# Performance work log

Hardware: AMD Instinct MI355X
Metric: run time of the kernel (lower is better)

The kernel has to match this reference:

```python
import jax, jax.numpy as jnp
import numpy as np

DIM = 4096
N_HEADS = 32
N_KV_HEADS = 8
HEAD_DIM = 128
WINDOW = 1024
SEQ = 2048
ROPE_THETA = 10000.0


def setup_inputs() -> dict:
    key = jax.random.key(0)
    ks = jax.random.split(key, 5)
    x = jax.random.normal(ks[0], (SEQ, DIM), dtype=jnp.float32)
    # torch nn.Linear weights are [out_features, in_features]
    wq = jax.random.normal(ks[1], (N_HEADS * HEAD_DIM, DIM), dtype=jnp.float32) * (DIM ** -0.5)
    wk = jax.random.normal(ks[2], (N_KV_HEADS * HEAD_DIM, DIM), dtype=jnp.float32) * (DIM ** -0.5)
    wv = jax.random.normal(ks[3], (N_KV_HEADS * HEAD_DIM, DIM), dtype=jnp.float32) * (DIM ** -0.5)
    wo = jax.random.normal(ks[4], (DIM, N_HEADS * HEAD_DIM), dtype=jnp.float32) * ((N_HEADS * HEAD_DIM) ** -0.5)
    # RoPE freqs: freqs_cis[t, i] = exp(1j * t * theta^(-2i/d)); store cos/sin
    inv_freq = ROPE_THETA ** (-jnp.arange(0, HEAD_DIM, 2, dtype=jnp.float32) / HEAD_DIM)  # [D/2]
    angles = jnp.arange(SEQ, dtype=jnp.float32)[:, None] * inv_freq[None, :]  # [S, D/2]
    return {"x": x, "wq": wq, "wk": wk, "wv": wv, "wo": wo,
            "cos": jnp.cos(angles), "sin": jnp.sin(angles)}


def _apply_rope(t, cos, sin):
    # t: [S, H, D]; cos/sin: [S, D/2] -> rotate consecutive pairs as complex mul
    S, H, D = t.shape
    tr = t.reshape(S, H, D // 2, 2)
    t0, t1 = tr[..., 0], tr[..., 1]
    c = cos[:, None, :]
    s = sin[:, None, :]
    out = jnp.stack([t0 * c - t1 * s, t0 * s + t1 * c], axis=-1)
    return out.reshape(S, H, D)


def reference(x, wq, wk, wv, wo, cos, sin):
    S = x.shape[0]
    repeats = N_HEADS // N_KV_HEADS
    scale = HEAD_DIM ** -0.5
    q = (x @ wq.T).reshape(S, N_HEADS, HEAD_DIM)
    k = (x @ wk.T).reshape(S, N_KV_HEADS, HEAD_DIM)
    v = (x @ wv.T).reshape(S, N_KV_HEADS, HEAD_DIM)
    q = _apply_rope(q, cos, sin)
    k = _apply_rope(k, cos, sin)
    # repeat_kv: repeat_interleave along head axis (GQA)
    k = jnp.repeat(k, repeats, axis=1)  # [S, H, D]
    v = jnp.repeat(v, repeats, axis=1)
    scores = jnp.einsum('qhd,khd->hqk', q, k) * scale  # [H, S, S]
    # sliding-window causal mask: attend to j in (i - WINDOW, i]
    i = jnp.arange(S)[:, None]
    j = jnp.arange(S)[None, :]
    allowed = (j <= i) & (i - j < WINDOW)  # [S, S]
    scores = jnp.where(allowed[None, :, :], scores, jnp.finfo(scores.dtype).min)
    probs = jax.nn.softmax(scores, axis=-1)
    out = jnp.einsum('hqk,khd->qhd', probs, v).reshape(S, N_HEADS * HEAD_DIM)
    return out @ wo.T
```

## Files before the change

kernel.cpp:

```cpp
#include <hip/hip_runtime.h>

#define DIM 4096
#define NH 32
#define NKV 8
#define HD 128
#define WINDOW 1024
#define SEQ 2048
#define QLD 6144

typedef unsigned int uint32;
typedef __attribute__((ext_vector_type(8))) short short8_t;
typedef __attribute__((ext_vector_type(8))) __bf16 bf16x8_t;
typedef __attribute__((ext_vector_type(4))) float floatx4_t;

__device__ __forceinline__ uint32 f2bf_bits(float f) {
  uint32 u = __builtin_bit_cast(uint32, f);
  return (u + 0x7fffu + ((u >> 16) & 1u)) >> 16;
}
__device__ __forceinline__ float bf2f(unsigned short b) {
  return __builtin_bit_cast(float, ((uint32)b) << 16);
}

template <class X, class Y> struct same_t { static constexpr bool v = false; };
template <class X> struct same_t<X, X> { static constexpr bool v = true; };

__device__ __forceinline__ void load_lds16(const unsigned short* g, unsigned short* l) {
  __builtin_amdgcn_global_load_lds((__attribute__((address_space(1))) void*)g,
                                   (__attribute__((address_space(3))) void*)l, 16, 0, 0);
}

template <typename TC, bool ROPE, int BM, int BN>
__global__ __launch_bounds__(512, 2) void gemm_pipe(const unsigned short* __restrict__ A,
                                                    const unsigned short* __restrict__ B,
                                                    TC* __restrict__ C, int N, int K,
                                                    const float* __restrict__ cosp,
                                                    const float* __restrict__ sinp,
                                                    int rope_ncols) {
  constexpr int BK = 32;
  constexpr int MI = BM / 32;
  constexpr int NJ = BN / 64;
  constexpr int IA = (BM * 64) / 8192;
  constexpr int IT = IA + 2;
  constexpr int AE = BM * BK;
  constexpr int BUFE = 14336;
  __shared__ unsigned short lds[3 * BUFE];

  const int tid = threadIdx.x;
  const int w = tid >> 6, lane = tid & 63;
  const int quad = lane >> 4, l16 = lane & 15;
  const int wm = w >> 2, wn = w & 3;
  const size_t m0 = (size_t)blockIdx.y * BM, n0 = (size_t)blockIdx.x * BN;

  const unsigned short* asrc[IA];
  const unsigned short* bsrc[2];
#pragma unroll
  for (int ii = 0; ii < IA; ii++) {
    const int rloc = ii * 128 + (tid >> 2);
    const int c = ((tid & 3) + 4 - ((rloc >> 1) & 3)) & 3;
    asrc[ii] = A + (m0 + rloc) * (size_t)K + c * 8;
  }
#pragma unroll
  for (int ii = 0; ii < 2; ii++) {
    const int r0 = ii ? (BN - 128) : 0;
    const int rloc = r0 + (tid >> 2);
    const int c = ((tid & 3) + 4 - ((rloc >> 1) & 3)) & 3;
    bsrc[ii] = B + (n0 + rloc) * (size_t)K + c * 8;
  }
  const int bdst1 = AE + (BN - 128) * BK;

  int aoff[MI], boff[NJ];
#pragma unroll
  for (int i = 0; i < MI; i++) {
    const int row = wm * (BM / 2) + i * 16 + l16;
    const int s = (quad + (row >> 1)) & 3;
    aoff[i] = row * BK + s * 8;
  }
#pragma unroll
  for (int j = 0; j < NJ; j++) {
    const int row = wn * (BN / 4) + j * 16 + l16;
    const int s = (quad + (row >> 1)) & 3;
    boff[j] = AE + row * BK + s * 8;
  }

  auto stage = [&](int kt, int bi) {
    unsigned short* buf = lds + bi * BUFE + w * 512;
    const size_t ko = (size_t)kt * BK;
#pragma unroll
    for (int ii = 0; ii < IA; ii++)
      load_lds16(asrc[ii] + ko, buf + ii * 4096);
    load_lds16(bsrc[0] + ko, buf + AE);
    load_lds16(bsrc[1] + ko, buf + bdst1);
  };

  floatx4_t acc[MI][NJ] = {};
  const int nt = K >> 5;

  stage(0, 0);
  stage(1, 1);
  int rb = 0;
  for (int t = 0; t < nt; t++) {
    int sb = rb + 2; if (sb >= 3) sb -= 3;
    if (t + 2 < nt) {
      stage(t + 2, sb);
      if constexpr (IT == 4) asm volatile("s_waitcnt vmcnt(8)" ::: "memory");
      else                   asm volatile("s_waitcnt vmcnt(6)" ::: "memory");
    } else if (t + 2 == nt) {
      if constexpr (IT == 4) asm volatile("s_waitcnt vmcnt(4)" ::: "memory");
      else                   asm volatile("s_waitcnt vmcnt(3)" ::: "memory");
    } else {
      asm volatile("s_waitcnt vmcnt(0)" ::: "memory");
    }
    __builtin_amdgcn_s_barrier();
    const unsigned short* buf = lds + rb * BUFE;
    bf16x8_t afr[MI], bfr[NJ];
#pragma unroll
    for (int i = 0; i < MI; i++)
      afr[i] = __builtin_bit_cast(bf16x8_t, *(const short8_t*)(buf + aoff[i]));
#pragma unroll
    for (int j = 0; j < NJ; j++)
      bfr[j] = __builtin_bit_cast(bf16x8_t, *(const short8_t*)(buf + boff[j]));
    asm volatile("s_waitcnt lgkmcnt(0)" ::: "memory");
    __builtin_amdgcn_s_barrier();
    __builtin_amdgcn_s_setprio(1);
#pragma unroll
    for (int i = 0; i < MI; i++)
#pragma unroll
      for (int j = 0; j < NJ; j++)
        acc[i][j] = __builtin_amdgcn_mfma_f32_16x16x32_bf16(afr[i], bfr[j], acc[i][j], 0, 0, 0);
    __builtin_amdgcn_s_setprio(0);
    rb = (rb == 2) ? 0 : rb + 1;
  }

#pragma unroll
  for (int i = 0; i < MI; i++)
#pragma unroll
    for (int j = 0; j < NJ; j++) {
      const int colb = (int)n0 + wn * (BN / 4) + j * 16;
      const bool do_rope = ROPE && (colb < rope_ncols);
#pragma unroll
      for (int r = 0; r < 4; r++) {
        size_t row = m0 + wm * (BM / 2) + i * 16 + quad * 4 + r;
        size_t col = n0 + wn * (BN / 4) + j * 16 + l16;
        float v = acc[i][j][r];
        if constexpr (ROPE) {
          if (do_rope) {
            float pv = __shfl_xor(v, 1);
            const int d = ((int)col & 127) >> 1;
            const float c = cosp[row * 64 + d];
            const float s = sinp[row * 64 + d];
            v = ((int)col & 1) ? (pv * s + v * c) : (v * c - pv * s);
          }
        }
        if constexpr (same_t<TC, float>::v)
          C[row * (size_t)N + col] = v;
        else
          C[row * (size_t)N + col] = (unsigned short)f2bf_bits(v);
      }
    }
}

__global__ __launch_bounds__(256) void cvt4_kernel(const float* __restrict__ s0,
                                                   const float* __restrict__ s1,
                                                   const float* __restrict__ s2,
                                                   const float* __restrict__ s3,
                                                   unsigned short* __restrict__ d0,
                                                   unsigned short* __restrict__ d1,
                                                   unsigned short* __restrict__ d2,
                                                   unsigned short* __restrict__ d3) {
  const int b = blockIdx.x;
  const float* src;
  unsigned short* dst;
  int rb;
  if (b < 4096)        { src = s0; dst = d0; rb = b; }
  else if (b < 12288)  { src = s1; dst = d1; rb = b - 4096; }
  else if (b < 14336)  { src = s2; dst = d2; rb = b - 12288; }
  else                 { src = s3; dst = d3; rb = b - 14336; }
  const int idx = rb * 256 + threadIdx.x;
  const float4* p = (const float4*)src + (size_t)idx * 2;
  float4 a = p[0], bb = p[1];
  uint32 w0 = f2bf_bits(a.x) | (f2bf_bits(a.y) << 16);
  uint32 w1 = f2bf_bits(a.z) | (f2bf_bits(a.w) << 16);
  uint32 w2 = f2bf_bits(bb.x) | (f2bf_bits(bb.y) << 16);
  uint32 w3 = f2bf_bits(bb.z) | (f2bf_bits(bb.w) << 16);
  ((uint4*)dst)[idx] = make_uint4(w0, w1, w2, w3);
}

__global__ __launch_bounds__(256) void epi_kernel(const float* __restrict__ wo,
                                                  unsigned short* __restrict__ wob,
                                                  const unsigned short* __restrict__ v,
                                                  unsigned short* __restrict__ vT) {
  __shared__ unsigned short t[64][72];
  const int b = blockIdx.x;
  const int tid = threadIdx.x;
  if (b < 8192) {
    const int idx = b * 256 + tid;
    const float4* p = (const float4*)wo + (size_t)idx * 2;
    float4 a = p[0], bb = p[1];
    uint32 w0 = f2bf_bits(a.x) | (f2bf_bits(a.y) << 16);
    uint32 w1 = f2bf_bits(a.z) | (f2bf_bits(a.w) << 16);
    uint32 w2 = f2bf_bits(bb.x) | (f2bf_bits(bb.y) << 16);
    uint32 w3 = f2bf_bits(bb.z) | (f2bf_bits(bb.w) << 16);
    ((uint4*)wob)[idx] = make_uint4(w0, w1, w2, w3);
    return;
  }
  const int bx = b - 8192;
  const int r0 = (bx & 15) * 64, s0 = (bx >> 4) * 64;
#pragma unroll
  for (int it = 0; it < 2; it++) {
    int f = it * 256 + tid;
    int si = f >> 3, cj = (f & 7) << 3;
    *(short8_t*)(&t[si][cj]) = *(const short8_t*)(v + (size_t)(s0 + si) * QLD + r0 + cj);
  }
  __syncthreads();
#pragma unroll
  for (int it = 0; it < 2; it++) {
    int f = it * 256 + tid;
    int ri = f >> 3, sj = (f & 7) << 3;
    short8_t o;
#pragma unroll
    for (int jj = 0; jj < 8; jj++) o[jj] = t[sj + jj][ri];
    *(short8_t*)(vT + (size_t)(r0 + ri) * SEQ + s0 + sj) = o;
  }
}

__global__ __launch_bounds__(512, 4) void attn_kernel(const unsigned short* __restrict__ qb,
                                                      const unsigned short* __restrict__ kb,
                                                      const unsigned short* __restrict__ vT,
                                                      unsigned short* __restrict__ attn_out) {
  const int h = blockIdx.x;
  const int qt = 15 - blockIdx.y;
  const int kvh = h >> 2;
  const int q0 = qt * 128;
  const int tid = threadIdx.x;
  const int w = tid >> 6, lane = tid & 63;
  const int quad = lane >> 4, l16 = lane & 15;
  const float SCALE = 0.08838834764831845f;

  __shared__ unsigned short Ks[64 * 128];
  __shared__ unsigned short VTs[128 * 64];
  __shared__ unsigned short PTs[8 * 16 * 72];

  unsigned short* pt = &PTs[w * 1152];

  const int krow = tid >> 4;
  const int kc16 = tid & 15;
  const int kgcol = (kc16 ^ (krow & 7)) << 3;
  const unsigned short* kgbase = kb + (size_t)krow * QLD + kvh * 128 + kgcol;
  const int vrow = tid >> 3;
  const int vc8 = tid & 7;
  const int vgcol = (vc8 ^ (vrow & 7)) << 3;
  const unsigned short* vgbase = vT + (size_t)(kvh * 128 + vrow) * 2048 + vgcol;
  unsigned short* ldsK = Ks + w * 512;
  unsigned short* ldsV = VTs + w * 512;

  bf16x8_t aq[4];
  {
    const unsigned short* qp = qb + (size_t)(q0 + w * 16 + l16) * QLD + h * 128 + quad * 8;
#pragma unroll
    for (int ks = 0; ks < 4; ks++)
      aq[ks] = __builtin_bit_cast(bf16x8_t, *(const short8_t*)(qp + ks * 32));
  }

  floatx4_t O[8] = {};
  float m_run[4], l_run[4];
#pragma unroll
  for (int r = 0; r < 4; r++) { m_run[r] = -3e38f; l_run[r] = 0.0f; }

  const int qmin = q0 + w * 16, qmax = qmin + 15;
  int kbeg = q0 - (WINDOW - 1); if (kbeg < 0) kbeg = 0;
  const int c0 = kbeg & ~63;
  const int nch = (q0 + 128 - c0) >> 6;
  const int sa = l16 & 7;

  for (int ci = 0; ci < nch; ci++) {
    const int kb0 = c0 + (ci << 6);
#pragma unroll
    for (int i = 0; i < 2; i++)
      load_lds16(kgbase + (size_t)(kb0 + i * 32) * QLD, ldsK + i * 4096);
#pragma unroll
    for (int i = 0; i < 2; i++)
      load_lds16(vgbase + kb0 + (size_t)(i * 64) * 2048, ldsV + i * 4096);
    __syncthreads();
    const bool alive = (kb0 <= qmax) && (kb0 + 63 >= qmin - (WINDOW - 1));
    if (alive) {
      floatx4_t S[4];
      __builtin_amdgcn_s_setprio(1);
#pragma unroll
      for (int j = 0; j < 4; j++) {
        floatx4_t acc = {};
        const int keyrow = j * 16 + l16;
#pragma unroll
        for (int ks = 0; ks < 4; ks++) {
          const int c16 = ((ks << 2) | quad) ^ sa;
          bf16x8_t bfk = __builtin_bit_cast(bf16x8_t,
              *(const short8_t*)(&Ks[keyrow * 128 + c16 * 8]));
          acc = __builtin_amdgcn_mfma_f32_16x16x32_bf16(aq[ks], bfk, acc, 0, 0, 0);
        }
        S[j] = acc;
      }
      __builtin_amdgcn_s_setprio(0);
      const bool need_mask = (kb0 + 63 > qmin) || (qmax - kb0 >= WINDOW);
      if (need_mask) {
#pragma unroll
        for (int j = 0; j < 4; j++) {
          const int key = kb0 + j * 16 + l16;
#pragma unroll
          for (int r = 0; r < 4; r++) {
            const int i = qmin + quad * 4 + r;
            const bool ok = (key <= i) && (i - key < WINDOW);
            S[j][r] = ok ? S[j][r] : -3e38f;
          }
        }
      }
      float mx[4], rs[4], alpha[4];
#pragma unroll
      for (int r = 0; r < 4; r++) {
        float m = S[0][r];
#pragma unroll
        for (int j = 1; j < 4; j++) m = fmaxf(m, S[j][r]);
#pragma unroll
        for (int d = 1; d < 16; d <<= 1) m = fmaxf(m, __shfl_xor(m, d, 16));
        mx[r] = fmaxf(m_run[r], m);
        alpha[r] = __expf(SCALE * (m_run[r] - mx[r]));
        m_run[r] = mx[r];
        rs[r] = 0.0f;
      }
#pragma unroll
      for (int j = 0; j < 4; j++) {
        float p[4];
#pragma unroll
        for (int r = 0; r < 4; r++) {
          const float sv = S[j][r];
          float e = __expf(SCALE * (sv - mx[r]));
          if (need_mask) e = (sv < -1e37f) ? 0.0f : e;
          p[r] = e;
          rs[r] += e;
        }
#pragma unroll
        for (int r = 0; r < 4; r++)
          pt[(quad * 4 + r) * 72 + j * 16 + l16] = (unsigned short)f2bf_bits(p[r]);
      }
#pragma unroll
      for (int r = 0; r < 4; r++) {
#pragma unroll
        for (int d = 1; d < 16; d <<= 1) rs[r] += __shfl_xor(rs[r], d, 16);
        l_run[r] = l_run[r] * alpha[r] + rs[r];
      }
#pragma unroll
      for (int nt = 0; nt < 8; nt++)
#pragma unroll
        for (int r = 0; r < 4; r++) O[nt][r] *= alpha[r];
      asm volatile("" ::: "memory");
      __builtin_amdgcn_s_setprio(1);
#pragma unroll
      for (int ks = 0; ks < 2; ks++) {
        bf16x8_t af = __builtin_bit_cast(bf16x8_t,
            *(const short8_t*)(&pt[l16 * 72 + ks * 32 + quad * 8]));
#pragma unroll
        for (int nt = 0; nt < 8; nt++) {
          const int c8 = (((ks << 2) | quad) ^ sa);
          bf16x8_t bfv = __builtin_bit_cast(bf16x8_t,
              *(const short8_t*)(&VTs[(nt * 16 + l16) * 64 + c8 * 8]));
          O[nt] = __builtin_amdgcn_mfma_f32_16x16x32_bf16(af, bfv, O[nt], 0, 0, 0);
        }
      }
      __builtin_amdgcn_s_setprio(0);
    }
    __syncthreads();
  }
  float inv_l[4];
#pragma unroll
  for (int r = 0; r < 4; r++) inv_l[r] = 1.0f / l_run[r];
#pragma unroll
  for (int nt = 0; nt < 8; nt++)
#pragma unroll
    for (int r = 0; r < 4; r++) {
      float v = O[nt][r] * inv_l[r];
      attn_out[(size_t)(qmin + quad * 4 + r) * 4096 + h * 128 + nt * 16 + l16] =
          (unsigned short)f2bf_bits(v);
    }
}

extern "C" void kernel_launch(void* const* d_in, const int* in_sizes, int n_in,
                              void* d_out, int out_size, void* d_ws, size_t ws_size,
                              hipStream_t stream) {
  (void)in_sizes; (void)n_in; (void)out_size; (void)ws_size;
  const float* x    = (const float*)d_in[0];
  const float* wq   = (const float*)d_in[1];
  const float* wk   = (const float*)d_in[2];
  const float* wv   = (const float*)d_in[3];
  const float* wo   = (const float*)d_in[4];
  const float* cosp = (const float*)d_in[5];
  const float* sinp = (const float*)d_in[6];
  float* out = (float*)d_out;
  char* ws = (char*)d_ws;

  unsigned short* wqkvb = (unsigned short*)(ws);
  unsigned short* wob   = (unsigned short*)(ws);
  unsigned short* vTb   = (unsigned short*)(ws + 33554432);
  unsigned short* xb    = (unsigned short*)(ws + 50331648);
  unsigned short* attnb = (unsigned short*)(ws + 50331648);
  unsigned short* qkvb  = (unsigned short*)(ws + 67108864);

  cvt4_kernel<<<16384, 256, 0, stream>>>(
      x, wq, wk, wv,
      xb, wqkvb, wqkvb + (size_t)4096 * 4096, wqkvb + (size_t)5120 * 4096);
  gemm_pipe<unsigned short, true, 256, 192><<<dim3(32, 8), 512, 0, stream>>>(
      xb, wqkvb, qkvb, QLD, DIM, cosp, sinp, 5120);
  epi_kernel<<<8704, 256, 0, stream>>>(wo, wob, qkvb + 5120, vTb);
  attn_kernel<<<dim3(NH, 16), 512, 0, stream>>>(qkvb, qkvb + 4096, vTb, attnb);
  gemm_pipe<float, false, 128, 256><<<dim3(16, 16), 512, 0, stream>>>(
      attnb, wob, out, 4096, DIM, nullptr, nullptr, 0);
}
```

Baseline: 477.2 us.

## Switch GEMM to BK=64 double-buffered pipeline with XOR-swizzled LDS layout

Rewrites the bf16 GEMM main loop to use a K-tile of 64 with two LDS buffers instead of a K-tile of 32 with three. Each 64-wide K-step is split into two MFMA sub-steps, and the LDS layout changes to an XOR-swizzled 8-chunk scheme to avoid bank conflicts. Fewer barriers per unit of K are intended to cut synchronisation overhead. In exchange, the next tile's prefetch is now issued only after compute, which shortens the load/compute overlap, and the s_setprio hints are removed.

```diff
diff --git a/kernel.cpp b/kernel.cpp
--- a/kernel.cpp
+++ b/kernel.cpp
@@ -30,20 +30,21 @@
 }
 
 template <typename TC, bool ROPE, int BM, int BN>
-__global__ __launch_bounds__(512, 2) void gemm_pipe(const unsigned short* __restrict__ A,
-                                                    const unsigned short* __restrict__ B,
-                                                    TC* __restrict__ C, int N, int K,
-                                                    const float* __restrict__ cosp,
-                                                    const float* __restrict__ sinp,
-                                                    int rope_ncols) {
-  constexpr int BK = 32;
+__global__ __launch_bounds__(512, 2) void gemm_pipe2(const unsigned short* __restrict__ A,
+                                                     const unsigned short* __restrict__ B,
+                                                     TC* __restrict__ C, int N, int K,
+                                                     const float* __restrict__ cosp,
+                                                     const float* __restrict__ sinp,
+                                                     int rope_ncols) {
+  constexpr int BK = 64;
   constexpr int MI = BM / 32;
   constexpr int NJ = BN / 64;
-  constexpr int IA = (BM * 64) / 8192;
-  constexpr int IT = IA + 2;
+  constexpr int IA = BM / 64;
+  constexpr int IB = BN / 64;
+  constexpr int IT = IA + IB;
   constexpr int AE = BM * BK;
-  constexpr int BUFE = 14336;
-  __shared__ unsigned short lds[3 * BUFE];
+  constexpr int BUFE = (BM + BN) * BK;
+  __shared__ unsigned short lds[2 * BUFE];
 
   const int tid = threadIdx.x;
   const int w = tid >> 6, lane = tid & 63;
@@ -51,84 +52,70 @@
   const int wm = w >> 2, wn = w & 3;
   const size_t m0 = (size_t)blockIdx.y * BM, n0 = (size_t)blockIdx.x * BN;
 
+  const int srow = tid >> 3;
+  const int schunk = ((tid & 7) ^ (srow & 7)) << 3;
   const unsigned short* asrc[IA];
-  const unsigned short* bsrc[2];
-#pragma unroll
-  for (int ii = 0; ii < IA; ii++) {
-    const int rloc = ii * 128 + (tid >> 2);
-    const int c = ((tid & 3) + 4 - ((rloc >> 1) & 3)) & 3;
-    asrc[ii] = A + (m0 + rloc) * (size_t)K + c * 8;
-  }
-#pragma unroll
-  for (int ii = 0; ii < 2; ii++) {
-    const int r0 = ii ? (BN - 128) : 0;
-    const int rloc = r0 + (tid >> 2);
-    const int c = ((tid & 3) + 4 - ((rloc >> 1) & 3)) & 3;
-    bsrc[ii] = B + (n0 + rloc) * (size_t)K + c * 8;
-  }
-  const int bdst1 = AE + (BN - 128) * BK;
-
-  int aoff[MI], boff[NJ];
-#pragma unroll
-  for (int i = 0; i < MI; i++) {
-    const int row = wm * (BM / 2) + i * 16 + l16;
-    const int s = (quad + (row >> 1)) & 3;
-    aoff[i] = row * BK + s * 8;
-  }
-#pragma unroll
-  for (int j = 0; j < NJ; j++) {
-    const int row = wn * (BN / 4) + j * 16 + l16;
-    const int s = (quad + (row >> 1)) & 3;
-    boff[j] = AE + row * BK + s * 8;
-  }
-
-  auto stage = [&](int kt, int bi) {
-    unsigned short* buf = lds + bi * BUFE + w * 512;
+  const unsigned short* bsrc[IB];
+#pragma unroll
+  for (int ii = 0; ii < IA; ii++)
+    asrc[ii] = A + (m0 + ii * 64 + srow) * (size_t)K + schunk;
+#pragma unroll
+  for (int ii = 0; ii < IB; ii++)
+    bsrc[ii] = B + (n0 + ii * 64 + srow) * (size_t)K + schunk;
+  const int w512 = w * 512;
+
+  auto stage = [&](int kt, int bsel) {
+    unsigned short* buf = lds + bsel * BUFE;
     const size_t ko = (size_t)kt * BK;
 #pragma unroll
     for (int ii = 0; ii < IA; ii++)
-      load_lds16(asrc[ii] + ko, buf + ii * 4096);
-    load_lds16(bsrc[0] + ko, buf + AE);
-    load_lds16(bsrc[1] + ko, buf + bdst1);
+      load_lds16(asrc[ii] + ko, buf + ii * 4096 + w512);
+#pragma unroll
+    for (int ii = 0; ii < IB; ii++)
+      load_lds16(bsrc[ii] + ko, buf + AE + ii * 4096 + w512);
   };
 
   floatx4_t acc[MI][NJ] = {};
-  const int nt = K >> 5;
+  const int sa = l16 & 7;
+  const int nt = K >> 6;
 
   stage(0, 0);
   stage(1, 1);
-  int rb = 0;
+
   for (int t = 0; t < nt; t++) {
-    int sb = rb + 2; if (sb >= 3) sb -= 3;
-    if (t + 2 < nt) {
-      stage(t + 2, sb);
-      if constexpr (IT == 4) asm volatile("s_waitcnt vmcnt(8)" ::: "memory");
+    if (t + 1 < nt) {
+      if constexpr (IT == 7) asm volatile("s_waitcnt vmcnt(7)" ::: "memory");
       else                   asm volatile("s_waitcnt vmcnt(6)" ::: "memory");
-    } else if (t + 2 == nt) {
-      if constexpr (IT == 4) asm volatile("s_waitcnt vmcnt(4)" ::: "memory");
-      else                   asm volatile("s_waitcnt vmcnt(3)" ::: "memory");
     } else {
       asm volatile("s_waitcnt vmcnt(0)" ::: "memory");
     }
     __builtin_amdgcn_s_barrier();
-    const unsigned short* buf = lds + rb * BUFE;
-    bf16x8_t afr[MI], bfr[NJ];
-#pragma unroll
-    for (int i = 0; i < MI; i++)
-      afr[i] = __builtin_bit_cast(bf16x8_t, *(const short8_t*)(buf + aoff[i]));
-#pragma unroll
-    for (int j = 0; j < NJ; j++)
-      bfr[j] = __builtin_bit_cast(bf16x8_t, *(const short8_t*)(buf + boff[j]));
+    asm volatile("" ::: "memory");
+    const unsigned short* buf = lds + (t & 1) * BUFE;
+#pragma unroll
+    for (int ks = 0; ks < 2; ks++) {
+      bf16x8_t afr[MI], bfr[NJ];
+      const int cs = (((ks << 2) | quad) ^ sa) << 3;
+#pragma unroll
+      for (int i = 0; i < MI; i++) {
+        const int row = wm * (BM / 2) + i * 16 + l16;
+        afr[i] = __builtin_bit_cast(bf16x8_t, *(const short8_t*)(buf + row * 64 + cs));
+      }
+#pragma unroll
+      for (int j = 0; j < NJ; j++) {
+        const int row = wn * (BN / 4) + j * 16 + l16;
+        bfr[j] = __builtin_bit_cast(bf16x8_t, *(const short8_t*)(buf + AE + row * 64 + cs));
+      }
+#pragma unroll
+      for (int i = 0; i < MI; i++)
+#pragma unroll
+        for (int j = 0; j < NJ; j++)
+          acc[i][j] = __builtin_amdgcn_mfma_f32_16x16x32_bf16(afr[i], bfr[j], acc[i][j], 0, 0, 0);
+    }
     asm volatile("s_waitcnt lgkmcnt(0)" ::: "memory");
     __builtin_amdgcn_s_barrier();
-    __builtin_amdgcn_s_setprio(1);
-#pragma unroll
-    for (int i = 0; i < MI; i++)
-#pragma unroll
-      for (int j = 0; j < NJ; j++)
-        acc[i][j] = __builtin_amdgcn_mfma_f32_16x16x32_bf16(afr[i], bfr[j], acc[i][j], 0, 0, 0);
-    __builtin_amdgcn_s_setprio(0);
-    rb = (rb == 2) ? 0 : rb + 1;
+    asm volatile("" ::: "memory");
+    if (t + 2 < nt) stage(t + 2, t & 1);
   }
 
 #pragma unroll
@@ -405,10 +392,10 @@
   cvt4_kernel<<<16384, 256, 0, stream>>>(
       x, wq, wk, wv,
       xb, wqkvb, wqkvb + (size_t)4096 * 4096, wqkvb + (size_t)5120 * 4096);
-  gemm_pipe<unsigned short, true, 256, 192><<<dim3(32, 8), 512, 0, stream>>>(
+  gemm_pipe2<unsigned short, true, 256, 192><<<dim3(32, 8), 512, 0, stream>>>(
       xb, wqkvb, qkvb, QLD, DIM, cosp, sinp, 5120);
   epi_kernel<<<8704, 256, 0, stream>>>(wo, wob, qkvb + 5120, vTb);
   attn_kernel<<<dim3(NH, 16), 512, 0, stream>>>(qkvb, qkvb + 4096, vTb, attnb);
-  gemm_pipe<float, false, 128, 256><<<dim3(16, 16), 512, 0, stream>>>(
+  gemm_pipe2<float, false, 128, 256><<<dim3(16, 16), 512, 0, stream>>>(
       attnb, wob, out, 4096, DIM, nullptr, nullptr, 0);
 }
```

Result: faster. 467.5 us (-2.0%).
